# Kernel optimization log

Measured on AMD Instinct MI355X. Metric: run time of the kernel, lower is better.

Reference implementation:

```python
import jax, jax.numpy as jnp
from jax import lax
import numpy as np

POOLING_COUNTS = [15, 8, 8, 8]
N = 128          # segment_num
GROUPS = 4       # GroupNorm groups
TOPK = 5
NMS_THRESH = 0.5
EPS = 1e-5


def _build_structure(pooling_counts, n):
    """Static (numpy) replication of SparseMaxPool's mask2d and pooling schedule."""
    mask2d = np.zeros((n, n), dtype=bool)
    mask2d[np.arange(n), np.arange(n)] = True
    kinds = ['k2'] * pooling_counts[0]
    for c in pooling_counts[1:]:
        kinds += ['k3'] + ['k2'] * (c - 1)
    steps, stride, offset, k = [], 1, 0, 0
    for c in pooling_counts:
        for _ in range(c):
            offset += stride
            i = np.arange(0, n - offset, stride)
            j = np.arange(offset, n, stride)
            mask2d[i, j] = True
            steps.append((kinds[k], i, j))
            k += 1
        stride *= 2
    return mask2d, steps


_MASK2D, _STEPS = _build_structure(POOLING_COUNTS, N)


def sparse_max_pool(x):
    # x: [B, D, N] -> map2d: [B, D, N, N]
    B, D, _ = x.shape
    d = np.arange(N)
    map2d = jnp.zeros((B, D, N, N), x.dtype).at[:, :, d, d].set(x)
    for kind, i, j in _STEPS:
        if kind == 'k2':      # MaxPool1d(kernel=2, stride=1)
            x = jnp.maximum(x[..., :-1], x[..., 1:])
        else:                 # MaxPool1d(kernel=3, stride=2)
            m = jnp.maximum(jnp.maximum(x[..., :-2], x[..., 1:-1]), x[..., 2:])
            x = m[..., ::2]
        map2d = map2d.at[:, :, i, j].set(x)
    return map2d


def group_norm(x, gamma, beta):
    B, C, H, W = x.shape
    xg = x.reshape(B, GROUPS, C // GROUPS, H, W)
    mu = xg.mean(axis=(2, 3, 4), keepdims=True)
    var = xg.var(axis=(2, 3, 4), keepdims=True)
    xn = ((xg - mu) * lax.rsqrt(var + EPS)).reshape(B, C, H, W)
    return xn * gamma[None, :, None, None] + beta[None, :, None, None]


def decode(map2d, conv1_w, gn_gamma, gn_beta, conv2_w, conv2_b):
    dn = ('NCHW', 'OIHW', 'NCHW')
    h = lax.conv_general_dilated(map2d, conv1_w, (1, 1), [(1, 1), (1, 1)], dimension_numbers=dn)
    h = jax.nn.relu(group_norm(h, gn_gamma, gn_beta))
    out = lax.conv_general_dilated(h, conv2_w, (1, 1), [(0, 0), (0, 0)], dimension_numbers=dn)
    return out + conv2_b[None, :, None, None]


def greedy_nms(moments, scores):
    # moments: [M, 2] (start, end); scores: [M]
    M = moments.shape[0]
    order = jnp.argsort(-scores)
    m = moments[order]
    starts, ends = m[:, 0], m[:, 1]
    ar = jnp.arange(M)

    def body(i, sup):
        inter = jnp.clip(jnp.minimum(ends, ends[i]) - jnp.maximum(starts, starts[i]), 0.0)
        union = jnp.maximum(ends, ends[i]) - jnp.minimum(starts, starts[i])
        iou = inter / union
        newly = (iou > NMS_THRESH) & (ar > i) & jnp.logical_not(sup[i])
        return sup | newly

    sup = lax.fori_loop(0, M - 1, body, jnp.zeros((M,), bool))
    keep = jnp.logical_not(sup)
    # first TOPK kept rows in sorted order (static shape)
    pri = jnp.where(keep, M - ar, 0)
    _, idx = lax.top_k(pri, TOPK)
    return m[idx]


def reference(fea, duration, conv1_w, gn_gamma, gn_beta, conv2_w, conv2_b):
    map2d = sparse_max_pool(fea)
    out = decode(map2d, conv1_w, gn_gamma, gn_beta, conv2_w, conv2_b)
    mask = jnp.asarray(_MASK2D, out.dtype)
    score2d = (jax.nn.sigmoid(out) * mask)[0, 0]           # [N, N]
    # score2d_to_moments_scores: nonzero of masked map == static nonzero of mask2d
    gi, gj = np.nonzero(_MASK2D)                            # row-major, matches torch.nonzero
    scores = score2d[gi, gj]                                # [M]
    dur = float(duration)
    moments = jnp.asarray(
        np.stack([gi * (dur / N), (gj + 1) * (dur / N)], axis=-1), jnp.float32
    )                                                       # [M, 2]
    return greedy_nms(moments, scores)                      # [TOPK, 2]


def setup_inputs() -> dict:
    key = jax.random.key(0)
    k0, k1, k2 = jax.random.split(key, 3)
    D = 768
    return {
        'fea': jax.random.normal(k0, (1, D, N), jnp.float32),
        'duration': 30,
        'conv1_w': jax.random.normal(k1, (D, D, 3, 3), jnp.float32) * 0.02,
        'gn_gamma': jnp.ones((D,), jnp.float32),
        'gn_beta': jnp.zeros((D,), jnp.float32),
        'conv2_w': jax.random.normal(k2, (1, D, 1, 1), jnp.float32) * 0.02,
        'conv2_b': jnp.zeros((1,), jnp.float32),
    }
```

## Files before the change

kernel.cpp:

```cpp
#include <hip/hip_runtime.h>
#include <math.h>

#define NPIX 128
#define MASKM 2548
#define NPAD 2560
#define MG   6912
#define KD   768

typedef __attribute__((ext_vector_type(8))) short bf16x8;
typedef __attribute__((ext_vector_type(4))) float f32x4;
typedef __attribute__((ext_vector_type(16))) float f32x16;
typedef __attribute__((ext_vector_type(8))) unsigned short ushort8;

static constexpr size_t OFF_QI   = 0;
static constexpr size_t OFF_QJ   = OFF_QI + NPAD * 4;
static constexpr size_t OFF_QIDX = OFF_QJ + NPAD * 4;
static constexpr size_t OFF_APIX = OFF_QIDX + 16384 * 4;
static constexpr size_t OFF_BAR  = OFF_APIX + 16384 * 4;
static constexpr size_t OFF_PART = OFF_BAR + 128 * 4;
static constexpr size_t OFF_SC   = OFF_PART + 512 * 8 * 8;
static constexpr size_t OFF_HM   = OFF_SC + NPAD * 4;
static constexpr size_t OFF_AH   = OFF_HM + (size_t)MASKM * KD * 4;
static constexpr size_t OFF_AL   = OFF_AH + (size_t)MG * KD * 2;
static constexpr size_t OFF_BH   = OFF_AL + (size_t)MG * KD * 2;
static constexpr size_t OFF_BL   = OFF_BH + (size_t)NPAD * KD * 2;
static constexpr size_t OFF_YT   = OFF_BL + (size_t)NPAD * KD * 2;

__device__ __forceinline__ unsigned short f2bf(float f) {
    unsigned u = __float_as_uint(f);
    u = u + 0x7FFFu + ((u >> 16) & 1u);
    return (unsigned short)(u >> 16);
}
__device__ __forceinline__ float bf2f(unsigned short h) {
    return __uint_as_float(((unsigned)h) << 16);
}

__device__ __forceinline__ bool mask_allowed(int i, int d) {
    if (d == 0) return true;
    if (d <= 15) return true;
    if (d <= 31) return (d >= 17) && ((d & 1) == 1) && ((i & 1) == 0);
    if (d <= 63) return (d >= 35) && ((d & 3) == 3) && ((i & 3) == 0);
    return (d >= 71) && ((d & 7) == 7) && ((i & 7) == 0);
}
__device__ __forceinline__ bool masked_ij(int i, int j) {
    return (j >= i) && (j < NPIX) && (i >= 0) && mask_allowed(i, j - i);
}

__device__ __forceinline__ int rank_to_d(int i, int r) {
    int rem = NPIX - i;
    int c1 = rem < 16 ? rem : 16;
    if (r < c1) return r;
    r -= c1;
    int h2 = (rem - 1) < 31 ? (rem - 1) : 31;
    int c2 = (((i & 1) == 0) && h2 >= 17) ? ((h2 - 17) >> 1) + 1 : 0;
    if (r < c2) return 17 + 2 * r;
    r -= c2;
    int h3 = (rem - 1) < 63 ? (rem - 1) : 63;
    int c3 = (((i & 3) == 0) && h3 >= 35) ? ((h3 - 35) >> 2) + 1 : 0;
    if (r < c3) return 35 + 4 * r;
    r -= c3;
    return 71 + 8 * r;
}

#define PREP_LDS 66816
#define PASTR 148

__global__ __launch_bounds__(256) void k_prep(const float* __restrict__ fea,
                                              const float* __restrict__ w1,
                                              int* __restrict__ qi, int* __restrict__ qj,
                                              int* __restrict__ qidx, int* __restrict__ apix,
                                              double* __restrict__ part, int* __restrict__ bar,
                                              unsigned short* __restrict__ Ah,
                                              unsigned short* __restrict__ Al,
                                              unsigned short* __restrict__ Bh,
                                              unsigned short* __restrict__ Bl) {
    extern __shared__ char smp[];
    int tid = threadIdx.x;
    int bid = blockIdx.x;

    if (bid < 64) {
        int* cnt = (int*)smp;
        int* startv = cnt + NPIX;
        if (tid < NPIX) {
            int c = 0;
            for (int d = 0; tid + d < NPIX; ++d) if (mask_allowed(tid, d)) ++c;
            cnt[tid] = c;
        }
        __syncthreads();
        if (tid == 0) {
            int s = 0;
            for (int r = 0; r < NPIX; ++r) { startv[r] = s; s += cnt[r]; }
        }
        __syncthreads();
        int p = bid * 256 + tid;
        int i = p >> 7, j = p & 127;
        int q = -1;
        if (masked_ij(i, j)) {
            int d = j - i, r = 0;
            for (int dd = 0; dd < d; ++dd) r += mask_allowed(i, dd) ? 1 : 0;
            q = startv[i] + r;
            qi[q] = i; qj[q] = j;
        }
        qidx[p] = q;
        int act = 0;
        #pragma unroll
        for (int dy = -1; dy <= 1; ++dy)
            #pragma unroll
            for (int dx = -1; dx <= 1; ++dx)
                if (masked_ij(i + dy, j + dx)) act = 1;
        apix[p] = act;
        if (bid == 0) {
            if (tid < 8) part[tid] = 0.0;
            if (tid >= 8 && tid < 12) bar[tid - 8] = 0;
        }
    } else if (bid < 112) {
        float* tab = (float*)smp;
        int* cnt = (int*)(smp + 65536);
        int* startv = (int*)(smp + 66048);
        int cb = bid - 64, c0 = cb * 16;
        if (tid < NPIX) {
            int c = 0;
            for (int d = 0; tid + d < NPIX; ++d) if (mask_allowed(tid, d)) ++c;
            cnt[tid] = c;
        }
        __syncthreads();
        if (tid == 0) {
            int s = 0;
            for (int r = 0; r < NPIX; ++r) { startv[r] = s; s += cnt[r]; }
            startv[NPIX] = s;
        }
        for (int idx = tid; idx < 16 * NPIX; idx += 256) {
            int c = idx >> 7, x = idx & 127;
            tab[(c * 8) * 128 + x] = fea[(size_t)(c0 + c) * NPIX + x];
        }
        __syncthreads();
        for (int lvl = 1; lvl < 8; ++lvl) {
            int half = 1 << (lvl - 1), full = 1 << lvl;
            for (int idx = tid; idx < 16 * NPIX; idx += 256) {
                int c = idx >> 7, x = idx & 127;
                if (x + full <= NPIX)
                    tab[(c * 8 + lvl) * 128 + x] =
                        fmaxf(tab[(c * 8 + lvl - 1) * 128 + x],
                              tab[(c * 8 + lvl - 1) * 128 + x + half]);
            }
            __syncthreads();
        }
        for (int q = tid; q < NPAD; q += 256) {
            ushort8 vh0 = {}, vh1 = {}, vl0 = {}, vl1 = {};
            if (q < MASKM) {
                int i = 0;
                #pragma unroll
                for (int s = 64; s >= 1; s >>= 1) {
                    int cand = i + s;
                    if (cand <= 127 && startv[cand] <= q) i = cand;
                }
                int d = rank_to_d(i, q - startv[i]);
                int j = i + d;
                int len = d + 1;
                int lvl = 31 - __clz(len);
                int x2 = j + 1 - (1 << lvl);
                #pragma unroll
                for (int c = 0; c < 8; ++c) {
                    float v = fmaxf(tab[(c * 8 + lvl) * 128 + i], tab[(c * 8 + lvl) * 128 + x2]);
                    unsigned short hh = f2bf(v);
                    vh0[c] = hh; vl0[c] = f2bf(v - bf2f(hh));
                }
                #pragma unroll
                for (int c = 0; c < 8; ++c) {
                    float v = fmaxf(tab[((c + 8) * 8 + lvl) * 128 + i], tab[((c + 8) * 8 + lvl) * 128 + x2]);
                    unsigned short hh = f2bf(v);
                    vh1[c] = hh; vl1[c] = f2bf(v - bf2f(hh));
                }
            }
            *(ushort8*)(Bh + (size_t)q * KD + c0)     = vh0;
            *(ushort8*)(Bh + (size_t)q * KD + c0 + 8) = vh1;
            *(ushort8*)(Bl + (size_t)q * KD + c0)     = vl0;
            *(ushort8*)(Bl + (size_t)q * KD + c0 + 8) = vl1;
        }
    } else {
        float* tile = (float*)smp;
        int pb = bid - 112;
        int co0 = (pb % 12) * 64, ci0 = (pb / 12) * 64;
        for (int s = 0; s < 4; ++s) {
            int cib = ci0 + s * 16;
            __syncthreads();
            for (int idx = tid; idx < 2304; idx += 256) {
                int row = idx / 36, c4 = idx % 36;
                float4 v = *(const float4*)(w1 + (size_t)(co0 + row) * MG + cib * 9 + c4 * 4);
                *(float4*)&tile[row * PASTR + c4 * 4] = v;
            }
            __syncthreads();
            for (int idx = tid; idx < 1152; idx += 256) {
                int tap = idx / 128;
                int rem = idx - tap * 128;
                int co = rem >> 1, half = rem & 1;
                ushort8 vh, vl;
                #pragma unroll
                for (int c = 0; c < 8; ++c) {
                    float v = tile[co * PASTR + (half * 8 + c) * 9 + tap];
                    unsigned short hi = f2bf(v);
                    vh[c] = hi;
                    vl[c] = f2bf(v - bf2f(hi));
                }
                size_t ob = (size_t)(tap * 768 + co0 + co) * KD + cib + half * 8;
                *(ushort8*)(Ah + ob) = vh;
                *(ushort8*)(Al + ob) = vl;
            }
        }
    }
}

#define BUFSZ   73728
#define SB_BH   32768

__global__ __launch_bounds__(512, 1) void k_gemm(const unsigned short* __restrict__ Ah,
                                                 const unsigned short* __restrict__ Al,
                                                 const unsigned short* __restrict__ Bh,
                                                 const unsigned short* __restrict__ Bl,
                                                 float* __restrict__ Yt) {
    extern __shared__ char sm[];
    int tid = threadIdx.x;
    int wave = tid >> 6, lane = tid & 63;

    int bid = (int)blockIdx.x;
    int xcd = bid & 7, loc = bid >> 3;
    int m0 = loc * 256, n0 = xcd * 320;

    int wm = (wave & 3) << 6, wn = (wave >> 2) * 160;
    int r32 = lane & 31, hi2 = lane >> 5;
    int rb  = (r32 >> 4) * 1024 + hi2 * 256 + (r32 & 15) * 16;
    int awb = (wm >> 4) * 1024 + rb;
    int bwb = (wn >> 4) * 1024 + rb;

    int lrow = lane & 15, lchk = lane >> 4;
    const unsigned short* sp[9];
    int so[9];
    #pragma unroll
    for (int s = 0; s < 9; ++s) {
        int gid = wave * 9 + s;
        const unsigned short* base;
        int row0, ldso;
        if (gid < 16)      { base = Ah; row0 = m0 + gid * 16;        ldso = gid * 1024; }
        else if (gid < 32) { base = Al; row0 = m0 + (gid - 16) * 16; ldso = 16384 + (gid - 16) * 1024; }
        else if (gid < 52) { base = Bh; row0 = n0 + (gid - 32) * 16; ldso = SB_BH + (gid - 32) * 1024; }
        else               { base = Bl; row0 = n0 + (gid - 52) * 16; ldso = SB_BH + 20480 + (gid - 52) * 1024; }
        sp[s] = base + (size_t)(row0 + lrow) * KD + lchk * 8;
        so[s] = ldso;
    }

    f32x16 acc[2][5] = {};
    char* CB = sm;
    char* NB = sm + BUFSZ;

    #define STAGE(DST, s, koff) __builtin_amdgcn_global_load_lds( \
        (const __attribute__((address_space(1))) unsigned int*)(sp[s] + (koff)), \
        (__attribute__((address_space(3))) unsigned int*)((DST) + so[s]), 16, 0, 0)
    #define ARD(hl, mf, ks) (*(const bf16x8*)(CB + (hl) * 16384 + awb + (mf) * 2048 + (ks) * 512))
    #define BRD(hl, nf, ks) (*(const bf16x8*)(CB + SB_BH + (hl) * 20480 + bwb + (nf) * 2048 + (ks) * 512))
    #define TRIP(mf, nf, xh, xl, yh, yl) \
        acc[mf][nf] = __builtin_amdgcn_mfma_f32_32x32x16_bf16(xh, yh, acc[mf][nf], 0, 0, 0); \
        acc[mf][nf] = __builtin_amdgcn_mfma_f32_32x32x16_bf16(xh, yl, acc[mf][nf], 0, 0, 0); \
        acc[mf][nf] = __builtin_amdgcn_mfma_f32_32x32x16_bf16(xl, yh, acc[mf][nf], 0, 0, 0);

    #pragma unroll
    for (int s = 0; s < 9; ++s) STAGE(CB, s, 0);
    __syncthreads();

    for (int t = 0; t < 24; ++t) {
        int kn = (t + 1) * 32;
        if (t < 23) {
            #pragma unroll
            for (int s = 0; s < 9; ++s) STAGE(NB, s, kn);
        }
        #pragma unroll
        for (int ks = 0; ks < 2; ++ks) {
            bf16x8 a0h = ARD(0, 0, ks), a0l = ARD(1, 0, ks);
            bf16x8 a1h = ARD(0, 1, ks), a1l = ARD(1, 1, ks);
            bf16x8 bxh = BRD(0, 0, ks), bxl = BRD(1, 0, ks);
            bf16x8 byh = BRD(0, 1, ks), byl = BRD(1, 1, ks);
            __builtin_amdgcn_s_setprio(1);
            TRIP(0, 0, a0h, a0l, bxh, bxl)
            TRIP(1, 0, a1h, a1l, bxh, bxl)
            __builtin_amdgcn_s_setprio(0);
            bxh = BRD(0, 2, ks); bxl = BRD(1, 2, ks);
            __builtin_amdgcn_s_setprio(1);
            TRIP(0, 1, a0h, a0l, byh, byl)
            TRIP(1, 1, a1h, a1l, byh, byl)
            __builtin_amdgcn_s_setprio(0);
            byh = BRD(0, 3, ks); byl = BRD(1, 3, ks);
            __builtin_amdgcn_s_setprio(1);
            TRIP(0, 2, a0h, a0l, bxh, bxl)
            TRIP(1, 2, a1h, a1l, bxh, bxl)
            __builtin_amdgcn_s_setprio(0);
            bxh = BRD(0, 4, ks); bxl = BRD(1, 4, ks);
            __builtin_amdgcn_s_setprio(1);
            TRIP(0, 3, a0h, a0l, byh, byl)
            TRIP(1, 3, a1h, a1l, byh, byl)
            TRIP(0, 4, a0h, a0l, bxh, bxl)
            TRIP(1, 4, a1h, a1l, bxh, bxl)
            __builtin_amdgcn_s_setprio(0);
        }
        __syncthreads();
        char* tmp = CB; CB = NB; NB = tmp;
    }

    #pragma unroll
    for (int mf = 0; mf < 2; ++mf)
        #pragma unroll
        for (int nf = 0; nf < 5; ++nf) {
            int n = n0 + wn + nf * 32 + r32;
            size_t rowb = (size_t)n * MG + m0 + wm + mf * 32 + 4 * hi2;
            #pragma unroll
            for (int g = 0; g < 4; ++g) {
                f32x4 v = { acc[mf][nf][g * 4 + 0], acc[mf][nf][g * 4 + 1],
                            acc[mf][nf][g * 4 + 2], acc[mf][nf][g * 4 + 3] };
                *(f32x4*)(Yt + rowb + 8 * g) = v;
            }
        }
    #undef STAGE
    #undef ARD
    #undef BRD
    #undef TRIP
}

__global__ __launch_bounds__(256) void k_gather(const float* __restrict__ Yt,
                                                const int* __restrict__ qidx,
                                                const int* __restrict__ apix,
                                                float* __restrict__ hm,
                                                double* __restrict__ part) {
    __shared__ double red1[256 * 4], red2[256 * 4];
    int tid = threadIdx.x;
    int wave = tid >> 6, lane = tid & 63;
    double a1[3] = {0, 0, 0}, a2[3] = {0, 0, 0};
    int gs[3];
    #pragma unroll
    for (int s = 0; s < 3; ++s) gs[s] = (64 * s + lane) / 48;

    for (int it = 0; it < 8; ++it) {
        int p = blockIdx.x * 32 + wave * 8 + it;
        if (!apix[p]) continue;
        int y = p >> 7, x = p & 127;
        float4 hv[3] = {};
        #pragma unroll
        for (int tap = 0; tap < 9; ++tap) {
            int i = y + tap / 3 - 1, j = x + tap % 3 - 1;
            if ((unsigned)i < 128u && (unsigned)j < 128u) {
                int q = qidx[i * NPIX + j];
                if (q >= 0) {
                    const float* yr = Yt + (size_t)q * MG + tap * 768 + lane * 4;
                    #pragma unroll
                    for (int s = 0; s < 3; ++s) {
                        float4 v = *(const float4*)(yr + s * 256);
                        hv[s].x += v.x; hv[s].y += v.y; hv[s].z += v.z; hv[s].w += v.w;
                    }
                }
            }
        }
        int qp = qidx[p];
        if (qp >= 0) {
            #pragma unroll
            for (int s = 0; s < 3; ++s)
                *(float4*)(hm + (size_t)qp * KD + s * 256 + lane * 4) = hv[s];
        }
        #pragma unroll
        for (int s = 0; s < 3; ++s) {
            a1[s] += (double)hv[s].x + (double)hv[s].y + (double)hv[s].z + (double)hv[s].w;
            a2[s] += (double)hv[s].x * hv[s].x + (double)hv[s].y * hv[s].y +
                     (double)hv[s].z * hv[s].z + (double)hv[s].w * hv[s].w;
        }
    }
    #pragma unroll
    for (int g = 0; g < 4; ++g) { red1[tid * 4 + g] = 0.0; red2[tid * 4 + g] = 0.0; }
    #pragma unroll
    for (int s = 0; s < 3; ++s) { red1[tid * 4 + gs[s]] = a1[s]; red2[tid * 4 + gs[s]] = a2[s]; }
    __syncthreads();
    if (tid < 8) {
        int g = tid & 3;
        double s = 0.0;
        if (tid < 4) { for (int i = 0; i < 256; ++i) s += red1[i * 4 + g]; }
        else         { for (int i = 0; i < 256; ++i) s += red2[i * 4 + g]; }
        atomicAdd(&part[tid], s);
    }
}

#define SNMS_LDS 44544

__global__ __launch_bounds__(256) void k_scorenms(const float* __restrict__ hm,
                                                  const double* __restrict__ part,
                                                  const float* __restrict__ gamma,
                                                  const float* __restrict__ beta,
                                                  const float* __restrict__ w2,
                                                  const float* __restrict__ b2,
                                                  float* __restrict__ scores,
                                                  const int* __restrict__ qi,
                                                  const int* __restrict__ qj,
                                                  const int* __restrict__ durp,
                                                  int* __restrict__ bar,
                                                  float* __restrict__ out) {
    extern __shared__ char smf[];
    int tid = threadIdx.x;
    int bid = (int)blockIdx.x;
    int lane = tid & 63;

    {
        float mu[4], rs[4];
        const double cnt = 192.0 * 16384.0;
        #pragma unroll
        for (int g = 0; g < 4; ++g) {
            double m = part[g] / cnt;
            double v = part[4 + g] / cnt - m * m;
            mu[g] = (float)m;
            rs[g] = (float)(1.0 / sqrt(v + 1e-5));
        }
        int q = bid * 4 + (tid >> 6);
        const float* hp = hm + (size_t)q * KD;
        float s = 0.f;
        for (int c = lane; c < KD; c += 64) {
            int g = c / 192;
            float v = (hp[c] - mu[g]) * rs[g] * gamma[c] + beta[c];
            s += fmaxf(v, 0.f) * w2[c];
        }
        for (int o = 32; o; o >>= 1) s += __shfl_down(s, o, 64);
        if (lane == 0) scores[q] = 1.f / (1.f + expf(-(s + b2[0])));
    }
    __syncthreads();
    if (tid == 0)
        __hip_atomic_fetch_add(&bar[2], 1, __ATOMIC_RELEASE, __HIP_MEMORY_SCOPE_AGENT);
    if (bid != 0) return;

    if (tid == 0) {
        while (__hip_atomic_load(&bar[2], __ATOMIC_RELAXED, __HIP_MEMORY_SCOPE_AGENT) < 637)
            __builtin_amdgcn_s_sleep(8);
        (void)__hip_atomic_load(&bar[2], __ATOMIC_ACQUIRE, __HIP_MEMORY_SCOPE_AGENT);
    }
    __syncthreads();

    {
        unsigned long long* key = (unsigned long long*)smf;
        float* ss = (float*)(smf + 20384);
        float* ee = (float*)(smf + 30576);
        unsigned char* st = (unsigned char*)(smf + 40768);
        unsigned long long* wm0 = (unsigned long long*)(smf + 43328);
        unsigned long long* wm1 = (unsigned long long*)(smf + 43360);
        __shared__ int sh_keeper, keepq[5];
        __shared__ float sh_s0, sh_e0;

        float delta = (float)(*durp) / 128.f;
        for (int i = tid; i < MASKM; i += 256) {
            unsigned sb = __float_as_uint(scores[i]);
            key[i] = ((unsigned long long)sb << 32) | (unsigned)(4095 - i);
            ss[i] = qi[i] * delta;
            ee[i] = (qj[i] + 1) * delta;
            st[i] = 0;
        }
        __syncthreads();
        for (int round = 0; round < 5; ++round) {
            unsigned long long b0 = 0, b1 = 0;
            for (int i = tid; i < MASKM; i += 256) {
                unsigned char s = st[i];
                unsigned long long k = key[i];
                if (s == 0) { if (k > b0) b0 = k; }
                else if (s == 1) { if (k > b1) b1 = k; }
            }
            for (int o = 32; o; o >>= 1) {
                unsigned lo0 = __shfl_down((unsigned)b0, o, 64);
                unsigned hi0 = __shfl_down((unsigned)(b0 >> 32), o, 64);
                unsigned long long u0 = ((unsigned long long)hi0 << 32) | lo0;
                unsigned lo1 = __shfl_down((unsigned)b1, o, 64);
                unsigned hi1 = __shfl_down((unsigned)(b1 >> 32), o, 64);
                unsigned long long u1 = ((unsigned long long)hi1 << 32) | lo1;
                if (u0 > b0) b0 = u0;
                if (u1 > b1) b1 = u1;
            }
            if ((tid & 63) == 0) { wm0[tid >> 6] = b0; wm1[tid >> 6] = b1; }
            __syncthreads();
            if (tid == 0) {
                unsigned long long B0 = 0, B1 = 0;
                for (int w = 0; w < 4; ++w) {
                    if (wm0[w] > B0) B0 = wm0[w];
                    if (wm1[w] > B1) B1 = wm1[w];
                }
                int keeper = (B0 != 0);
                unsigned long long B = keeper ? B0 : B1;
                int q = 4095 - (int)(B & 0xFFFFFFFFull);
                st[q] = keeper ? 2 : 3;
                sh_keeper = keeper;
                sh_s0 = ss[q]; sh_e0 = ee[q];
                keepq[round] = q;
            }
            __syncthreads();
            if (sh_keeper) {
                float s0 = sh_s0, e0 = sh_e0;
                for (int i = tid; i < MASKM; i += 256) {
                    if (st[i] == 0) {
                        float inter = fminf(ee[i], e0) - fmaxf(ss[i], s0);
                        if (inter > 0.f) {
                            float uni = fmaxf(ee[i], e0) - fminf(ss[i], s0);
                            if (inter / uni > 0.5f) st[i] = 1;
                        }
                    }
                }
            }
            __syncthreads();
        }
        if (tid < 5) { out[tid * 2] = ss[keepq[tid]]; out[tid * 2 + 1] = ee[keepq[tid]]; }
    }
}

extern "C" void kernel_launch(void* const* d_in, const int* in_sizes, int n_in,
                              void* d_out, int out_size, void* d_ws, size_t ws_size,
                              hipStream_t stream) {
    const float* fea   = (const float*)d_in[0];
    const int*   dur   = (const int*)d_in[1];
    const float* w1    = (const float*)d_in[2];
    const float* gamma = (const float*)d_in[3];
    const float* beta  = (const float*)d_in[4];
    const float* w2    = (const float*)d_in[5];
    const float* b2    = (const float*)d_in[6];
    float* out = (float*)d_out;

    char* ws = (char*)d_ws;
    int*    qi     = (int*)(ws + OFF_QI);
    int*    qj     = (int*)(ws + OFF_QJ);
    int*    qidx   = (int*)(ws + OFF_QIDX);
    int*    apix   = (int*)(ws + OFF_APIX);
    int*    bar    = (int*)(ws + OFF_BAR);
    double* part   = (double*)(ws + OFF_PART);
    float*  scores = (float*)(ws + OFF_SC);
    float*  hm     = (float*)(ws + OFF_HM);
    unsigned short* AhU = (unsigned short*)(ws + OFF_AH);
    unsigned short* AlU = (unsigned short*)(ws + OFF_AL);
    unsigned short* BhU = (unsigned short*)(ws + OFF_BH);
    unsigned short* BlU = (unsigned short*)(ws + OFF_BL);
    float*  Yt     = (float*)(ws + OFF_YT);

    static bool attr_set = false;
    if (!attr_set) {
        hipFuncSetAttribute((const void*)k_prep,
                            hipFuncAttributeMaxDynamicSharedMemorySize, PREP_LDS);
        hipFuncSetAttribute((const void*)k_gemm,
                            hipFuncAttributeMaxDynamicSharedMemorySize, 2 * BUFSZ);
        hipFuncSetAttribute((const void*)k_scorenms,
                            hipFuncAttributeMaxDynamicSharedMemorySize, SNMS_LDS);
        attr_set = true;
    }

    k_prep<<<256, 256, PREP_LDS, stream>>>(fea, w1, qi, qj, qidx, apix, part, bar,
                                           AhU, AlU, BhU, BlU);
    k_gemm<<<216, 512, 2 * BUFSZ, stream>>>(AhU, AlU, BhU, BlU, Yt);
    k_gather<<<512, 256, 0, stream>>>(Yt, qidx, apix, hm, part);
    k_scorenms<<<637, 256, SNMS_LDS, stream>>>(hm, part, gamma, beta, w2, b2,
                                               scores, qi, qj, dur, bar, out);
}
```

Baseline: 273.5 us.

## Interleave global-to-LDS staging with MFMA phases using intra-iteration barriers

The GEMM main loop no longer issues all nine global_load_lds stages at the top of each K-step. The stages are now spread across the two k-sub-steps and two compute phases, with raw s_barrier calls keeping the waves in lockstep so LDS reads, async loads and MFMA clusters alternate. The aim is to smooth memory issue and overlap it with matrix work, in the style of a ping-pong schedule. The extra barriers add synchronization cost, and the extra B fragment registers (bz) raise register pressure.

```diff
diff --git a/kernel.cpp b/kernel.cpp
--- a/kernel.cpp
+++ b/kernel.cpp
@@ -261,6 +261,7 @@
         acc[mf][nf] = __builtin_amdgcn_mfma_f32_32x32x16_bf16(xh, yh, acc[mf][nf], 0, 0, 0); \
         acc[mf][nf] = __builtin_amdgcn_mfma_f32_32x32x16_bf16(xh, yl, acc[mf][nf], 0, 0, 0); \
         acc[mf][nf] = __builtin_amdgcn_mfma_f32_32x32x16_bf16(xl, yh, acc[mf][nf], 0, 0, 0);
+    #define RBAR __builtin_amdgcn_s_barrier()
 
     #pragma unroll
     for (int s = 0; s < 9; ++s) STAGE(CB, s, 0);
@@ -268,38 +269,47 @@
 
     for (int t = 0; t < 24; ++t) {
         int kn = (t + 1) * 32;
-        if (t < 23) {
-            #pragma unroll
-            for (int s = 0; s < 9; ++s) STAGE(NB, s, kn);
-        }
+        bool stg = (t < 23);
+        bf16x8 a0h, a0l, a1h, a1l, bxh, bxl, byh, byl;
+
         #pragma unroll
         for (int ks = 0; ks < 2; ++ks) {
-            bf16x8 a0h = ARD(0, 0, ks), a0l = ARD(1, 0, ks);
-            bf16x8 a1h = ARD(0, 1, ks), a1l = ARD(1, 1, ks);
-            bf16x8 bxh = BRD(0, 0, ks), bxl = BRD(1, 0, ks);
-            bf16x8 byh = BRD(0, 1, ks), byl = BRD(1, 1, ks);
+            a0h = ARD(0, 0, ks); a0l = ARD(1, 0, ks);
+            a1h = ARD(0, 1, ks); a1l = ARD(1, 1, ks);
+            bxh = BRD(0, 0, ks); bxl = BRD(1, 0, ks);
+            byh = BRD(0, 1, ks); byl = BRD(1, 1, ks);
+            if (stg) {
+                if (ks == 0) { STAGE(NB, 0, kn); STAGE(NB, 1, kn); STAGE(NB, 2, kn); }
+                else         { STAGE(NB, 5, kn); STAGE(NB, 6, kn); }
+            }
+            RBAR;
             __builtin_amdgcn_s_setprio(1);
             TRIP(0, 0, a0h, a0l, bxh, bxl)
             TRIP(1, 0, a1h, a1l, bxh, bxl)
-            __builtin_amdgcn_s_setprio(0);
-            bxh = BRD(0, 2, ks); bxl = BRD(1, 2, ks);
-            __builtin_amdgcn_s_setprio(1);
             TRIP(0, 1, a0h, a0l, byh, byl)
             TRIP(1, 1, a1h, a1l, byh, byl)
             __builtin_amdgcn_s_setprio(0);
+            RBAR;
+
+            bxh = BRD(0, 2, ks); bxl = BRD(1, 2, ks);
             byh = BRD(0, 3, ks); byl = BRD(1, 3, ks);
+            bf16x8 bzh = BRD(0, 4, ks), bzl = BRD(1, 4, ks);
+            if (stg) {
+                if (ks == 0) { STAGE(NB, 3, kn); STAGE(NB, 4, kn); }
+                else         { STAGE(NB, 7, kn); STAGE(NB, 8, kn); }
+            }
+            RBAR;
             __builtin_amdgcn_s_setprio(1);
             TRIP(0, 2, a0h, a0l, bxh, bxl)
             TRIP(1, 2, a1h, a1l, bxh, bxl)
-            __builtin_amdgcn_s_setprio(0);
-            bxh = BRD(0, 4, ks); bxl = BRD(1, 4, ks);
-            __builtin_amdgcn_s_setprio(1);
             TRIP(0, 3, a0h, a0l, byh, byl)
             TRIP(1, 3, a1h, a1l, byh, byl)
-            TRIP(0, 4, a0h, a0l, bxh, bxl)
-            TRIP(1, 4, a1h, a1l, bxh, bxl)
+            TRIP(0, 4, a0h, a0l, bzh, bzl)
+            TRIP(1, 4, a1h, a1l, bzh, bzl)
             __builtin_amdgcn_s_setprio(0);
-        }
+            if (ks == 0) RBAR;
+        }
+
         __syncthreads();
         char* tmp = CB; CB = NB; NB = tmp;
     }
@@ -321,6 +331,7 @@
     #undef ARD
     #undef BRD
     #undef TRIP
+    #undef RBAR
 }
 
 __global__ __launch_bounds__(256) void k_gather(const float* __restrict__ Yt,
```

Result: faster. 265.5 us (-2.9%).
